# Optimization experiments

Hardware: AMD Instinct MI355X
Metric: run time of the kernel (lower is better)

Reference implementation:

```python
import jax, jax.numpy as jnp
import numpy as np

NEG_SLOPE = 0.2  # DGL GATConv default negative_slope


def gat_conv(x, W, attn_l, attn_r, bias, src, dst, n_nodes):
    """DGL-style GATConv. x:[N,F_in], W:[F_in,H*D], attn_l/attn_r/bias:[H,D].
    Returns [N,H,D]."""
    H, D = attn_l.shape
    feat = (x @ W).reshape(n_nodes, H, D)            # projected features
    el = jnp.sum(feat * attn_l, axis=-1)              # [N,H]
    er = jnp.sum(feat * attn_r, axis=-1)              # [N,H]
    e = jax.nn.leaky_relu(el[src] + er[dst], NEG_SLOPE)  # [E,H] per-edge score
    # edge softmax over incoming edges of each dst node (numerically stable)
    m = jax.ops.segment_max(e, dst, num_segments=n_nodes)   # [N,H]
    a = jnp.exp(e - m[dst])
    denom = jax.ops.segment_sum(a, dst, num_segments=n_nodes)
    alpha = a / denom[dst]                            # [E,H]
    msg = feat[src] * alpha[..., None]                # [E,H,D]
    out = jax.ops.segment_sum(msg, dst, num_segments=n_nodes)  # [N,H,D]
    return out + bias


def setup_inputs() -> dict:
    key = jax.random.key(0)
    ks = jax.random.split(key, 12)
    N, E = 50000, 800000
    F_in, D1, H1, F_out = 128, 32, 4, 64
    h = jax.random.normal(ks[0], (N, F_in), dtype=jnp.float32)
    src = jax.random.randint(ks[1], (E,), 0, N, dtype=jnp.int32)
    dst = jax.random.randint(ks[2], (E,), 0, N, dtype=jnp.int32)
    s1 = 1.0 / np.sqrt(F_in)
    s2 = 1.0 / np.sqrt(H1 * D1)
    W1 = jax.random.normal(ks[3], (F_in, H1 * D1), dtype=jnp.float32) * s1
    al1 = jax.random.normal(ks[4], (H1, D1), dtype=jnp.float32) * s1
    ar1 = jax.random.normal(ks[5], (H1, D1), dtype=jnp.float32) * s1
    b1 = jnp.zeros((H1, D1), dtype=jnp.float32)
    W2 = jax.random.normal(ks[6], (H1 * D1, 1 * F_out), dtype=jnp.float32) * s2
    al2 = jax.random.normal(ks[7], (1, F_out), dtype=jnp.float32) * s2
    ar2 = jax.random.normal(ks[8], (1, F_out), dtype=jnp.float32) * s2
    b2 = jnp.zeros((1, F_out), dtype=jnp.float32)
    return {"h": h, "src": src, "dst": dst,
            "W1": W1, "al1": al1, "ar1": ar1, "b1": b1,
            "W2": W2, "al2": al2, "ar2": ar2, "b2": b2}


def reference(h, src, dst, W1, al1, ar1, b1, W2, al2, ar2, b2):
    N = h.shape[0]
    x = gat_conv(h, W1, al1, ar1, b1, src, dst, N)   # [N,H,D]
    x = jax.nn.relu(x.reshape(N, -1))                # flatten heads + ReLU
    # dropout(p=0.2) is identity in eval mode
    x = gat_conv(x, W2, al2, ar2, b2, src, dst, N)   # [N,1,F_out]
    return x.squeeze(1)
```

## Files before the change

kernel.cpp:

```cpp
#include <hip/hip_runtime.h>

#define NEG_SLOPE 0.2f
#define CH 4096
#define DCAP 2048

__device__ inline unsigned short f2bf(float f) {
    unsigned u = __float_as_uint(f);
    unsigned r = (u + 0x7FFFu + ((u >> 16) & 1u)) >> 16;
    return (unsigned short)r;
}
__device__ inline float bf2f(unsigned short s) {
    return __uint_as_float(((unsigned)s) << 16);
}
__device__ inline void wave_lds_fence() {
    asm volatile("s_waitcnt lgkmcnt(0)" ::: "memory");
}

__global__ void zerob_kernel(int* __restrict__ p, int n) {
    int i = blockIdx.x * blockDim.x + threadIdx.x;
    if (i < n) p[i] = 0;
}

__global__ __launch_bounds__(256) void bucketA_kernel(const int* __restrict__ dst,
                                                      int* __restrict__ bucket_cnt,
                                                      int E, int NB) {
    __shared__ int lh[1024];
    const int tid = threadIdx.x;
    for (int i = tid; i < 1024; i += 256) lh[i] = 0;
    __syncthreads();
    const int base = blockIdx.x * CH;
    const int cnt = min(CH, E - base);
    for (int i = tid; i < cnt; i += 256) atomicAdd(&lh[dst[base + i] >> 6], 1);
    __syncthreads();
    for (int b = tid; b < NB; b += 256)
        if (lh[b]) atomicAdd(&bucket_cnt[b], lh[b]);
}

__global__ __launch_bounds__(1024) void bucketB_kernel(const int* __restrict__ bucket_cnt,
                                                       int* __restrict__ bucket_base,
                                                       int* __restrict__ bucket_cursor,
                                                       int* __restrict__ row_start,
                                                       int N, int NB, int E) {
    __shared__ int sh[1024];
    const int tid = threadIdx.x;
    int v = (tid < NB) ? bucket_cnt[tid] : 0;
    sh[tid] = v;
    __syncthreads();
    for (int off = 1; off < 1024; off <<= 1) {
        int t = (tid >= off) ? sh[tid - off] : 0;
        __syncthreads();
        sh[tid] += t;
        __syncthreads();
    }
    int ex = sh[tid] - v;
    if (tid < NB) {
        bucket_base[tid] = ex;
        bucket_cursor[tid] = ex;
    }
    if (tid == NB - 1) bucket_base[NB] = ex + v;
    if (tid == 0) row_start[N] = E;
}

__global__ __launch_bounds__(256) void csrC_gemm1_kernel(
    const int* __restrict__ src, const int* __restrict__ dst,
    int* __restrict__ bucket_cursor, unsigned* __restrict__ tmp, int E, int NB,
    int nchunks, const float* __restrict__ h, const float* __restrict__ W1,
    const float* __restrict__ al1, const float* __restrict__ ar1,
    unsigned short* __restrict__ feat1b, float* __restrict__ el1,
    float* __restrict__ er1, int N) {
    __shared__ __align__(16) int smem[8448];
    const int tid = threadIdx.x;
    if ((int)blockIdx.x < nchunks) {
        int* lh = smem;
        int* lex = smem + 1024;
        int* lcur = smem + 2048;
        int* gbase_sh = smem + 3072;
        int* psum = smem + 4096;
        unsigned* sortedv = (unsigned*)(smem + 4352);
        const int base_e = blockIdx.x * CH;
        const int cnt_e = min(CH, E - base_e);
        for (int i = tid; i < 1024; i += 256) lh[i] = 0;
        __syncthreads();
        for (int i = tid; i < cnt_e; i += 256) atomicAdd(&lh[dst[base_e + i] >> 6], 1);
        __syncthreads();
        int s0 = lh[tid * 4], s1 = lh[tid * 4 + 1], s2 = lh[tid * 4 + 2], s3 = lh[tid * 4 + 3];
        int tot = s0 + s1 + s2 + s3;
        psum[tid] = tot;
        __syncthreads();
        for (int off = 1; off < 256; off <<= 1) {
            int t = (tid >= off) ? psum[tid - off] : 0;
            __syncthreads();
            psum[tid] += t;
            __syncthreads();
        }
        int ebase = psum[tid] - tot;
        lex[tid * 4] = ebase;
        lex[tid * 4 + 1] = ebase + s0;
        lex[tid * 4 + 2] = ebase + s0 + s1;
        lex[tid * 4 + 3] = ebase + s0 + s1 + s2;
        __syncthreads();
        for (int b = tid; b < NB; b += 256) {
            int c = lh[b];
            gbase_sh[b] = c ? atomicAdd(&bucket_cursor[b], c) : 0;
            lcur[b] = 0;
        }
        __syncthreads();
        for (int i = tid; i < cnt_e; i += 256) {
            int e = base_e + i;
            int d = dst[e];
            unsigned b = (unsigned)d >> 6;
            int r = atomicAdd(&lcur[b], 1);
            sortedv[lex[b] + r] =
                (b << 22) | ((unsigned)(d & 63) << 16) | (unsigned)(src[e] & 0xFFFF);
        }
        __syncthreads();
        for (int i = tid; i < cnt_e; i += 256) {
            unsigned v = sortedv[i];
            int b = v >> 22;
            tmp[gbase_sh[b] + (i - lex[b])] = v;
        }
    } else {
        float* xs = (float*)smem;
        const int row0 = ((int)blockIdx.x - nchunks) * 64;
        {
            const float4* s4 = (const float4*)h;
            float4* d4 = (float4*)xs;
            int base4 = row0 * 32;
            int tot4 = N * 32;
            for (int i = tid; i < 2048; i += 256)
                if (base4 + i < tot4) d4[i] = s4[base4 + i];
        }
        __syncthreads();
        const int lane = tid & 31;
        const int c0 = lane * 4;
        const int r0 = (tid >> 5) * 8;
        float acc[8][4] = {};
#pragma unroll 4
        for (int k = 0; k < 128; ++k) {
            float4 w = *(const float4*)(W1 + k * 128 + c0);
#pragma unroll
            for (int r = 0; r < 8; ++r) {
                float x = xs[(r0 + r) * 128 + k];
                acc[r][0] = fmaf(x, w.x, acc[r][0]);
                acc[r][1] = fmaf(x, w.y, acc[r][1]);
                acc[r][2] = fmaf(x, w.z, acc[r][2]);
                acc[r][3] = fmaf(x, w.w, acc[r][3]);
            }
        }
        float4 alv = *(const float4*)(al1 + c0);
        float4 arv = *(const float4*)(ar1 + c0);
#pragma unroll
        for (int r = 0; r < 8; ++r) {
            int row = row0 + r0 + r;
            if (row < N) {
                ushort4 fb;
                fb.x = f2bf(acc[r][0]);
                fb.y = f2bf(acc[r][1]);
                fb.z = f2bf(acc[r][2]);
                fb.w = f2bf(acc[r][3]);
                *(ushort4*)(feat1b + (size_t)row * 128 + c0) = fb;
                float pl = acc[r][0] * alv.x + acc[r][1] * alv.y + acc[r][2] * alv.z +
                           acc[r][3] * alv.w;
                float pr = acc[r][0] * arv.x + acc[r][1] * arv.y + acc[r][2] * arv.z +
                           acc[r][3] * arv.w;
#pragma unroll
                for (int off = 4; off >= 1; off >>= 1) {
                    pl += __shfl_xor(pl, off, 32);
                    pr += __shfl_xor(pr, off, 32);
                }
                if ((lane & 7) == 0) {
                    el1[row * 4 + (lane >> 3)] = pl;
                    er1[row * 4 + (lane >> 3)] = pr;
                }
            }
        }
    }
}

__global__ __launch_bounds__(64) void bucketD_kernel(const unsigned* __restrict__ tmp,
                                                     const int* __restrict__ bucket_base,
                                                     int* __restrict__ srcs,
                                                     int* __restrict__ row_start,
                                                     int N, int NB) {
    __shared__ unsigned sval[DCAP];
    __shared__ int ssrc[DCAP];
    __shared__ int dh[64], dex[64], dcur[64];
    const int b = blockIdx.x;
    const int tid = threadIdx.x;
    const int gb = bucket_base[b], ge = bucket_base[b + 1];
    const int cnt = ge - gb;
    dh[tid] = 0;
    __syncthreads();
    if (cnt <= DCAP) {
        for (int i = tid; i < cnt; i += 64) {
            unsigned v = tmp[gb + i];
            sval[i] = v;
            atomicAdd(&dh[(v >> 16) & 63], 1);
        }
        __syncthreads();
        int v = dh[tid], inc = v;
        for (int off = 1; off < 64; off <<= 1) {
            int t = __shfl_up(inc, off, 64);
            if (tid >= off) inc += t;
        }
        int ex = inc - v;
        dex[tid] = ex;
        dcur[tid] = 0;
        __syncthreads();
        for (int i = tid; i < cnt; i += 64) {
            unsigned val = sval[i];
            int dl = (val >> 16) & 63;
            int r = atomicAdd(&dcur[dl], 1);
            ssrc[dex[dl] + r] = (int)(val & 0xFFFFu);
        }
        __syncthreads();
        for (int i = tid; i < cnt; i += 64) srcs[gb + i] = ssrc[i];
        int dglob = b * 64 + tid;
        if (dglob < N) row_start[dglob] = gb + ex;
    } else {
        for (int i = tid; i < cnt; i += 64) atomicAdd(&dh[(tmp[gb + i] >> 16) & 63], 1);
        __syncthreads();
        int v = dh[tid], inc = v;
        for (int off = 1; off < 64; off <<= 1) {
            int t = __shfl_up(inc, off, 64);
            if (tid >= off) inc += t;
        }
        int ex = inc - v;
        dex[tid] = ex;
        dcur[tid] = 0;
        __syncthreads();
        for (int i = tid; i < cnt; i += 64) {
            unsigned val = tmp[gb + i];
            int dl = (val >> 16) & 63;
            int r = atomicAdd(&dcur[dl], 1);
            srcs[gb + dex[dl] + r] = (int)(val & 0xFFFFu);
        }
        int dglob = b * 64 + tid;
        if (dglob < N) row_start[dglob] = gb + ex;
    }
}

__global__ __launch_bounds__(256) void gemm2_fused(const float* __restrict__ out1,
                                                   const float* __restrict__ W2,
                                                   const float* __restrict__ al2,
                                                   const float* __restrict__ ar2,
                                                   unsigned short* __restrict__ feat2b,
                                                   float* __restrict__ el2,
                                                   float* __restrict__ er2, int N) {
    __shared__ float xs[128 * 128];
    const int tid = threadIdx.x;
    const int row0 = blockIdx.x * 128;
    {
        const float4* s4 = (const float4*)out1;
        float4* d4 = (float4*)xs;
        int base4 = row0 * 32;
        int tot4 = N * 32;
        for (int i = tid; i < 4096; i += 256)
            if (base4 + i < tot4) {
                float4 v = s4[base4 + i];
                v.x = v.x > 0.f ? v.x : 0.f;
                v.y = v.y > 0.f ? v.y : 0.f;
                v.z = v.z > 0.f ? v.z : 0.f;
                v.w = v.w > 0.f ? v.w : 0.f;
                d4[i] = v;
            }
    }
    __syncthreads();
    const int lane = tid & 15;
    const int c0 = lane * 4;
    const int r0 = (tid >> 4) * 8;
    float acc[8][4] = {};
#pragma unroll 4
    for (int k = 0; k < 128; ++k) {
        float4 w = *(const float4*)(W2 + k * 64 + c0);
#pragma unroll
        for (int r = 0; r < 8; ++r) {
            float x = xs[(r0 + r) * 128 + k];
            acc[r][0] = fmaf(x, w.x, acc[r][0]);
            acc[r][1] = fmaf(x, w.y, acc[r][1]);
            acc[r][2] = fmaf(x, w.z, acc[r][2]);
            acc[r][3] = fmaf(x, w.w, acc[r][3]);
        }
    }
    float4 alv = *(const float4*)(al2 + c0);
    float4 arv = *(const float4*)(ar2 + c0);
#pragma unroll
    for (int r = 0; r < 8; ++r) {
        int row = row0 + r0 + r;
        if (row < N) {
            ushort4 fb;
            fb.x = f2bf(acc[r][0]);
            fb.y = f2bf(acc[r][1]);
            fb.z = f2bf(acc[r][2]);
            fb.w = f2bf(acc[r][3]);
            *(ushort4*)(feat2b + (size_t)row * 64 + c0) = fb;
            float pl = acc[r][0] * alv.x + acc[r][1] * alv.y + acc[r][2] * alv.z +
                       acc[r][3] * alv.w;
            float pr = acc[r][0] * arv.x + acc[r][1] * arv.y + acc[r][2] * arv.z +
                       acc[r][3] * arv.w;
#pragma unroll
            for (int off = 8; off >= 1; off >>= 1) {
                pl += __shfl_xor(pl, off, 16);
                pr += __shfl_xor(pr, off, 16);
            }
            if (lane == 0) {
                el2[row] = pl;
                er2[row] = pr;
            }
        }
    }
}

__global__ __launch_bounds__(256) void gather1_kernel(const int* __restrict__ row_start,
                                                      const int* __restrict__ srcs,
                                                      const float* __restrict__ el1,
                                                      const float* __restrict__ er1,
                                                      const unsigned short* __restrict__ feat1b,
                                                      const float* __restrict__ b1,
                                                      float* __restrict__ out1, int N) {
    __shared__ int s_sh[4][64];
    __shared__ float a_sh[4][256];
    const int tid = threadIdx.x;
    const int w = tid >> 6;
    const int lane = tid & 63;
    const int d = blockIdx.x * 4 + w;
    if (d >= N) return;
    const int beg = row_start[d], end = row_start[d + 1];
    const int half = lane >> 5;
    const int l32 = lane & 31;
    const int c0 = l32 * 4;
    const int h = l32 >> 3;
    float4 er4 = *(const float4*)(er1 + (size_t)d * 4);
    float acc0 = 0.f, acc1 = 0.f, acc2 = 0.f, acc3 = 0.f;
    float bcc0 = 0.f, bcc1 = 0.f, bcc2 = 0.f, bcc3 = 0.f;
    float den = 0.f;
    for (int k0 = beg; k0 < end; k0 += 64) {
        const int M = min(64, end - k0);
        if (lane < M) {
            int s = srcs[k0 + lane];
            s_sh[w][lane] = s;
            float4 el4 = *(const float4*)(el1 + (size_t)s * 4);
            float v0 = el4.x + er4.x;
            float v1 = el4.y + er4.y;
            float v2 = el4.z + er4.z;
            float v3 = el4.w + er4.w;
            v0 = v0 > 0.f ? v0 : NEG_SLOPE * v0;
            v1 = v1 > 0.f ? v1 : NEG_SLOPE * v1;
            v2 = v2 > 0.f ? v2 : NEG_SLOPE * v2;
            v3 = v3 > 0.f ? v3 : NEG_SLOPE * v3;
            a_sh[w][lane * 4 + 0] = __expf(v0);
            a_sh[w][lane * 4 + 1] = __expf(v1);
            a_sh[w][lane * 4 + 2] = __expf(v2);
            a_sh[w][lane * 4 + 3] = __expf(v3);
        }
        wave_lds_fence();
        int e = half;
        for (; e + 2 < M; e += 4) {
            int s0 = s_sh[w][e], s1 = s_sh[w][e + 2];
            float a0 = a_sh[w][e * 4 + h];
            float a1 = a_sh[w][(e + 2) * 4 + h];
            ushort4 f0 = *(const ushort4*)(feat1b + (size_t)s0 * 128 + c0);
            ushort4 f1 = *(const ushort4*)(feat1b + (size_t)s1 * 128 + c0);
            den += a0 + a1;
            acc0 = fmaf(bf2f(f0.x), a0, acc0);
            acc1 = fmaf(bf2f(f0.y), a0, acc1);
            acc2 = fmaf(bf2f(f0.z), a0, acc2);
            acc3 = fmaf(bf2f(f0.w), a0, acc3);
            bcc0 = fmaf(bf2f(f1.x), a1, bcc0);
            bcc1 = fmaf(bf2f(f1.y), a1, bcc1);
            bcc2 = fmaf(bf2f(f1.z), a1, bcc2);
            bcc3 = fmaf(bf2f(f1.w), a1, bcc3);
        }
        if (e < M) {
            int s0 = s_sh[w][e];
            float a0 = a_sh[w][e * 4 + h];
            ushort4 f0 = *(const ushort4*)(feat1b + (size_t)s0 * 128 + c0);
            den += a0;
            acc0 = fmaf(bf2f(f0.x), a0, acc0);
            acc1 = fmaf(bf2f(f0.y), a0, acc1);
            acc2 = fmaf(bf2f(f0.z), a0, acc2);
            acc3 = fmaf(bf2f(f0.w), a0, acc3);
        }
        wave_lds_fence();
    }
    acc0 += bcc0;
    acc1 += bcc1;
    acc2 += bcc2;
    acc3 += bcc3;
    acc0 += __shfl_xor(acc0, 32, 64);
    acc1 += __shfl_xor(acc1, 32, 64);
    acc2 += __shfl_xor(acc2, 32, 64);
    acc3 += __shfl_xor(acc3, 32, 64);
    den += __shfl_xor(den, 32, 64);
    if (half == 0) {
        float inv = (end > beg) ? 1.f / den : 0.f;
        float4 bv = *(const float4*)(b1 + c0);
        *(float4*)(out1 + (size_t)d * 128 + c0) =
            make_float4(acc0 * inv + bv.x, acc1 * inv + bv.y,
                        acc2 * inv + bv.z, acc3 * inv + bv.w);
    }
}

__global__ __launch_bounds__(256) void gather2_kernel(const int* __restrict__ row_start,
                                                      const int* __restrict__ srcs,
                                                      const float* __restrict__ el2,
                                                      const float* __restrict__ er2,
                                                      const unsigned short* __restrict__ feat2b,
                                                      const float* __restrict__ b2,
                                                      float* __restrict__ out2, int N) {
    __shared__ int s_sh[4][64];
    __shared__ float a_sh[4][64];
    const int tid = threadIdx.x;
    const int w = tid >> 6;
    const int lane = tid & 63;
    const int d = blockIdx.x * 4 + w;
    if (d >= N) return;
    const int beg = row_start[d], end = row_start[d + 1];
    const int half = lane >> 5;
    const int l32 = lane & 31;
    const int c0 = l32 * 2;
    const float er_d = er2[d];
    float acc0 = 0.f, acc1 = 0.f, bcc0 = 0.f, bcc1 = 0.f, den = 0.f;
    for (int k0 = beg; k0 < end; k0 += 64) {
        const int M = min(64, end - k0);
        if (lane < M) {
            int s = srcs[k0 + lane];
            s_sh[w][lane] = s;
            float v = el2[s] + er_d;
            v = v > 0.f ? v : NEG_SLOPE * v;
            a_sh[w][lane] = __expf(v);
        }
        wave_lds_fence();
        int e = half;
        for (; e + 2 < M; e += 4) {
            int s0 = s_sh[w][e], s1 = s_sh[w][e + 2];
            float a0 = a_sh[w][e], a1 = a_sh[w][e + 2];
            ushort2 f0 = *(const ushort2*)(feat2b + (size_t)s0 * 64 + c0);
            ushort2 f1 = *(const ushort2*)(feat2b + (size_t)s1 * 64 + c0);
            den += a0 + a1;
            acc0 = fmaf(bf2f(f0.x), a0, acc0);
            acc1 = fmaf(bf2f(f0.y), a0, acc1);
            bcc0 = fmaf(bf2f(f1.x), a1, bcc0);
            bcc1 = fmaf(bf2f(f1.y), a1, bcc1);
        }
        if (e < M) {
            int s0 = s_sh[w][e];
            float a0 = a_sh[w][e];
            ushort2 f0 = *(const ushort2*)(feat2b + (size_t)s0 * 64 + c0);
            den += a0;
            acc0 = fmaf(bf2f(f0.x), a0, acc0);
            acc1 = fmaf(bf2f(f0.y), a0, acc1);
        }
        wave_lds_fence();
    }
    acc0 += bcc0;
    acc1 += bcc1;
    acc0 += __shfl_xor(acc0, 32, 64);
    acc1 += __shfl_xor(acc1, 32, 64);
    den += __shfl_xor(den, 32, 64);
    if (half == 0) {
        float inv = (end > beg) ? 1.f / den : 0.f;
        *(float2*)(out2 + (size_t)d * 64 + c0) =
            make_float2(acc0 * inv + b2[c0], acc1 * inv + b2[c0 + 1]);
    }
}

extern "C" void kernel_launch(void* const* d_in, const int* in_sizes, int n_in,
                              void* d_out, int out_size, void* d_ws, size_t ws_size,
                              hipStream_t stream) {
    const float* h   = (const float*)d_in[0];
    const int*   src = (const int*)d_in[1];
    const int*   dst = (const int*)d_in[2];
    const float* W1  = (const float*)d_in[3];
    const float* al1 = (const float*)d_in[4];
    const float* ar1 = (const float*)d_in[5];
    const float* b1  = (const float*)d_in[6];
    const float* W2  = (const float*)d_in[7];
    const float* al2 = (const float*)d_in[8];
    const float* ar2 = (const float*)d_in[9];
    const float* b2  = (const float*)d_in[10];

    const int N = in_sizes[0] / 128;
    const int E = in_sizes[1];
    const int NB = (N + 63) >> 6;

    char* ws = (char*)d_ws;
    size_t off = 0;
    auto alloc = [&](size_t elems) -> void* {
        void* p = (void*)(ws + off);
        off += ((elems * 4 + 255) / 256) * 256;
        return p;
    };
    int* bucket_cnt    = (int*)alloc(NB);
    int* bucket_base   = (int*)alloc(NB + 1);
    int* bucket_cursor = (int*)alloc(NB);
    unsigned* tmp      = (unsigned*)alloc(E);
    int* srcs          = (int*)alloc(E);
    int* row_start     = (int*)alloc(N + 1);
    float* el1   = (float*)alloc((size_t)N * 4);
    float* er1   = (float*)alloc((size_t)N * 4);
    unsigned short* feat1b = (unsigned short*)alloc((size_t)N * 64);
    float* out1  = (float*)alloc((size_t)N * 128);
    float* el2   = (float*)alloc(N);
    float* er2   = (float*)alloc(N);
    unsigned short* feat2b = (unsigned short*)alloc((size_t)N * 32);
    float* out2  = (float*)d_out;

    const int nchunks = (E + CH - 1) / CH;
    const int gemm1_blocks = (N + 63) / 64;

    zerob_kernel<<<(NB + 255) / 256, 256, 0, stream>>>(bucket_cnt, NB);
    bucketA_kernel<<<nchunks, 256, 0, stream>>>(dst, bucket_cnt, E, NB);
    bucketB_kernel<<<1, 1024, 0, stream>>>(bucket_cnt, bucket_base, bucket_cursor,
                                           row_start, N, NB, E);
    csrC_gemm1_kernel<<<nchunks + gemm1_blocks, 256, 0, stream>>>(
        src, dst, bucket_cursor, tmp, E, NB, nchunks, h, W1, al1, ar1, feat1b, el1,
        er1, N);
    bucketD_kernel<<<NB, 64, 0, stream>>>(tmp, bucket_base, srcs, row_start, N, NB);

    gather1_kernel<<<(N + 3) / 4, 256, 0, stream>>>(row_start, srcs, el1, er1, feat1b,
                                                    b1, out1, N);

    gemm2_fused<<<(N + 127) / 128, 256, 0, stream>>>(out1, W2, al2, ar2, feat2b, el2,
                                                     er2, N);
    gather2_kernel<<<(N + 3) / 4, 256, 0, stream>>>(row_start, srcs, el2, er2, feat2b,
                                                    b2, out2, N);
}
```

Before: 231.9 us.

## Store layer-1 output as bf16 with fused ReLU, widen bucketD, use memset

gather1 now applies ReLU and writes its 128-wide output as bf16 instead of fp32, and gemm2 reads and unpacks the bf16 rows. This halves the intermediate write and read traffic but adds rounding error to the second layer's input. bucketD now runs 256 threads per block instead of 64, so each bucket's edges are processed by more threads. The zeroing kernel is replaced by hipMemsetAsync.

```diff
diff --git a/kernel.cpp b/kernel.cpp
--- a/kernel.cpp
+++ b/kernel.cpp
@@ -14,11 +14,6 @@
 }
 __device__ inline void wave_lds_fence() {
     asm volatile("s_waitcnt lgkmcnt(0)" ::: "memory");
-}
-
-__global__ void zerob_kernel(int* __restrict__ p, int n) {
-    int i = blockIdx.x * blockDim.x + threadIdx.x;
-    if (i < n) p[i] = 0;
 }
 
 __global__ __launch_bounds__(256) void bucketA_kernel(const int* __restrict__ dst,
@@ -177,11 +172,11 @@
     }
 }
 
-__global__ __launch_bounds__(64) void bucketD_kernel(const unsigned* __restrict__ tmp,
-                                                     const int* __restrict__ bucket_base,
-                                                     int* __restrict__ srcs,
-                                                     int* __restrict__ row_start,
-                                                     int N, int NB) {
+__global__ __launch_bounds__(256) void bucketD_kernel(const unsigned* __restrict__ tmp,
+                                                      const int* __restrict__ bucket_base,
+                                                      int* __restrict__ srcs,
+                                                      int* __restrict__ row_start,
+                                                      int N, int NB) {
     __shared__ unsigned sval[DCAP];
     __shared__ int ssrc[DCAP];
     __shared__ int dh[64], dex[64], dcur[64];
@@ -189,58 +184,60 @@
     const int tid = threadIdx.x;
     const int gb = bucket_base[b], ge = bucket_base[b + 1];
     const int cnt = ge - gb;
-    dh[tid] = 0;
+    if (tid < 64) dh[tid] = 0;
     __syncthreads();
     if (cnt <= DCAP) {
-        for (int i = tid; i < cnt; i += 64) {
+        for (int i = tid; i < cnt; i += 256) {
             unsigned v = tmp[gb + i];
             sval[i] = v;
             atomicAdd(&dh[(v >> 16) & 63], 1);
         }
         __syncthreads();
-        int v = dh[tid], inc = v;
-        for (int off = 1; off < 64; off <<= 1) {
-            int t = __shfl_up(inc, off, 64);
-            if (tid >= off) inc += t;
-        }
-        int ex = inc - v;
-        dex[tid] = ex;
-        dcur[tid] = 0;
-        __syncthreads();
-        for (int i = tid; i < cnt; i += 64) {
+        if (tid < 64) {
+            int v = dh[tid], inc = v;
+            for (int off = 1; off < 64; off <<= 1) {
+                int t = __shfl_up(inc, off, 64);
+                if (tid >= off) inc += t;
+            }
+            dex[tid] = inc - v;
+            dcur[tid] = 0;
+            int dglob = b * 64 + tid;
+            if (dglob < N) row_start[dglob] = gb + inc - v;
+        }
+        __syncthreads();
+        for (int i = tid; i < cnt; i += 256) {
             unsigned val = sval[i];
             int dl = (val >> 16) & 63;
             int r = atomicAdd(&dcur[dl], 1);
             ssrc[dex[dl] + r] = (int)(val & 0xFFFFu);
         }
         __syncthreads();
-        for (int i = tid; i < cnt; i += 64) srcs[gb + i] = ssrc[i];
-        int dglob = b * 64 + tid;
-        if (dglob < N) row_start[dglob] = gb + ex;
+        for (int i = tid; i < cnt; i += 256) srcs[gb + i] = ssrc[i];
     } else {
-        for (int i = tid; i < cnt; i += 64) atomicAdd(&dh[(tmp[gb + i] >> 16) & 63], 1);
-        __syncthreads();
-        int v = dh[tid], inc = v;
-        for (int off = 1; off < 64; off <<= 1) {
-            int t = __shfl_up(inc, off, 64);
-            if (tid >= off) inc += t;
-        }
-        int ex = inc - v;
-        dex[tid] = ex;
-        dcur[tid] = 0;
-        __syncthreads();
-        for (int i = tid; i < cnt; i += 64) {
+        for (int i = tid; i < cnt; i += 256) atomicAdd(&dh[(tmp[gb + i] >> 16) & 63], 1);
+        __syncthreads();
+        if (tid < 64) {
+            int v = dh[tid], inc = v;
+            for (int off = 1; off < 64; off <<= 1) {
+                int t = __shfl_up(inc, off, 64);
+                if (tid >= off) inc += t;
+            }
+            dex[tid] = inc - v;
+            dcur[tid] = 0;
+            int dglob = b * 64 + tid;
+            if (dglob < N) row_start[dglob] = gb + inc - v;
+        }
+        __syncthreads();
+        for (int i = tid; i < cnt; i += 256) {
             unsigned val = tmp[gb + i];
             int dl = (val >> 16) & 63;
             int r = atomicAdd(&dcur[dl], 1);
             srcs[gb + dex[dl] + r] = (int)(val & 0xFFFFu);
         }
-        int dglob = b * 64 + tid;
-        if (dglob < N) row_start[dglob] = gb + ex;
-    }
-}
-
-__global__ __launch_bounds__(256) void gemm2_fused(const float* __restrict__ out1,
+    }
+}
+
+__global__ __launch_bounds__(256) void gemm2_fused(const unsigned short* __restrict__ out1b,
                                                    const float* __restrict__ W2,
                                                    const float* __restrict__ al2,
                                                    const float* __restrict__ ar2,
@@ -251,18 +248,21 @@
     const int tid = threadIdx.x;
     const int row0 = blockIdx.x * 128;
     {
-        const float4* s4 = (const float4*)out1;
-        float4* d4 = (float4*)xs;
-        int base4 = row0 * 32;
-        int tot4 = N * 32;
-        for (int i = tid; i < 4096; i += 256)
-            if (base4 + i < tot4) {
-                float4 v = s4[base4 + i];
-                v.x = v.x > 0.f ? v.x : 0.f;
-                v.y = v.y > 0.f ? v.y : 0.f;
-                v.z = v.z > 0.f ? v.z : 0.f;
-                v.w = v.w > 0.f ? v.w : 0.f;
-                d4[i] = v;
+        const uint4* s8 = (const uint4*)out1b;
+        int base8 = row0 * 16;
+        int tot8 = N * 16;
+        for (int i = tid; i < 2048; i += 256)
+            if (base8 + i < tot8) {
+                uint4 v = s8[base8 + i];
+                float* o = xs + i * 8;
+                o[0] = bf2f((unsigned short)(v.x & 0xFFFF));
+                o[1] = bf2f((unsigned short)(v.x >> 16));
+                o[2] = bf2f((unsigned short)(v.y & 0xFFFF));
+                o[3] = bf2f((unsigned short)(v.y >> 16));
+                o[4] = bf2f((unsigned short)(v.z & 0xFFFF));
+                o[5] = bf2f((unsigned short)(v.z >> 16));
+                o[6] = bf2f((unsigned short)(v.w & 0xFFFF));
+                o[7] = bf2f((unsigned short)(v.w >> 16));
             }
     }
     __syncthreads();
@@ -317,7 +317,8 @@
                                                       const float* __restrict__ er1,
                                                       const unsigned short* __restrict__ feat1b,
                                                       const float* __restrict__ b1,
-                                                      float* __restrict__ out1, int N) {
+                                                      unsigned short* __restrict__ out1b,
+                                                      int N) {
     __shared__ int s_sh[4][64];
     __shared__ float a_sh[4][256];
     const int tid = threadIdx.x;
@@ -395,9 +396,16 @@
     if (half == 0) {
         float inv = (end > beg) ? 1.f / den : 0.f;
         float4 bv = *(const float4*)(b1 + c0);
-        *(float4*)(out1 + (size_t)d * 128 + c0) =
-            make_float4(acc0 * inv + bv.x, acc1 * inv + bv.y,
-                        acc2 * inv + bv.z, acc3 * inv + bv.w);
+        float r0v = fmaxf(acc0 * inv + bv.x, 0.f);
+        float r1v = fmaxf(acc1 * inv + bv.y, 0.f);
+        float r2v = fmaxf(acc2 * inv + bv.z, 0.f);
+        float r3v = fmaxf(acc3 * inv + bv.w, 0.f);
+        ushort4 o;
+        o.x = f2bf(r0v);
+        o.y = f2bf(r1v);
+        o.z = f2bf(r2v);
+        o.w = f2bf(r3v);
+        *(ushort4*)(out1b + (size_t)d * 128 + c0) = o;
     }
 }
 
@@ -500,7 +508,7 @@
     float* el1   = (float*)alloc((size_t)N * 4);
     float* er1   = (float*)alloc((size_t)N * 4);
     unsigned short* feat1b = (unsigned short*)alloc((size_t)N * 64);
-    float* out1  = (float*)alloc((size_t)N * 128);
+    unsigned short* out1b  = (unsigned short*)alloc((size_t)N * 64);
     float* el2   = (float*)alloc(N);
     float* er2   = (float*)alloc(N);
     unsigned short* feat2b = (unsigned short*)alloc((size_t)N * 32);
@@ -509,19 +517,19 @@
     const int nchunks = (E + CH - 1) / CH;
     const int gemm1_blocks = (N + 63) / 64;
 
-    zerob_kernel<<<(NB + 255) / 256, 256, 0, stream>>>(bucket_cnt, NB);
+    hipMemsetAsync(bucket_cnt, 0, (size_t)NB * 4, stream);
     bucketA_kernel<<<nchunks, 256, 0, stream>>>(dst, bucket_cnt, E, NB);
     bucketB_kernel<<<1, 1024, 0, stream>>>(bucket_cnt, bucket_base, bucket_cursor,
                                            row_start, N, NB, E);
     csrC_gemm1_kernel<<<nchunks + gemm1_blocks, 256, 0, stream>>>(
         src, dst, bucket_cursor, tmp, E, NB, nchunks, h, W1, al1, ar1, feat1b, el1,
         er1, N);
-    bucketD_kernel<<<NB, 64, 0, stream>>>(tmp, bucket_base, srcs, row_start, N, NB);
+    bucketD_kernel<<<NB, 256, 0, stream>>>(tmp, bucket_base, srcs, row_start, N, NB);
 
     gather1_kernel<<<(N + 3) / 4, 256, 0, stream>>>(row_start, srcs, el1, er1, feat1b,
-                                                    b1, out1, N);
-
-    gemm2_fused<<<(N + 127) / 128, 256, 0, stream>>>(out1, W2, al2, ar2, feat2b, el2,
+                                                    b1, out1b, N);
+
+    gemm2_fused<<<(N + 127) / 128, 256, 0, stream>>>(out1b, W2, al2, ar2, feat2b, el2,
                                                      er2, N);
     gather2_kernel<<<(N + 3) / 4, 256, 0, stream>>>(row_start, srcs, el2, er2, feat2b,
                                                     b2, out2, N);
```

Result: faster. 222.5 us (-4.1%).
